# Optimization experiments

Hardware: AMD Instinct MI355X
Metric: run time of the kernel (lower is better)

Reference implementation:

```python
import jax, jax.numpy as jnp
import numpy as np

N_NODES = 100000
N_EDGES = 600000
IN_SIZE = 128
NUM_HEADS = 8
OUT_DIM = 16  # out_size // num_heads = 128 // 8
NEG_SLOPE = 0.2


def setup_inputs() -> dict:
    key = jax.random.key(0)
    k1, k2, k3, k4, k5, k6, k7 = jax.random.split(key, 7)
    h = jax.random.normal(k1, (N_NODES, IN_SIZE), dtype=jnp.float32)
    o = jax.random.normal(k2, (N_NODES, NUM_HEADS * OUT_DIM), dtype=jnp.float32)
    # scale params for numerical sanity of exp() in edge softmax
    W = jax.random.normal(k3, (IN_SIZE, NUM_HEADS * OUT_DIM), dtype=jnp.float32) * 0.05
    attn_l = jax.random.normal(k4, (NUM_HEADS, OUT_DIM), dtype=jnp.float32) * 0.05
    attn_r = jax.random.normal(k5, (NUM_HEADS, OUT_DIM), dtype=jnp.float32) * 0.05
    src = jax.random.randint(k6, (N_EDGES,), 0, N_NODES, dtype=jnp.int64)
    dst = jax.random.randint(k7, (N_EDGES,), 0, N_NODES, dtype=jnp.int64)
    return {"h": h, "o": o, "W": W, "attn_l": attn_l, "attn_r": attn_r,
            "src": src, "dst": dst}


def reference(h, o, W, attn_l, attn_r, src, dst):
    N = h.shape[0]
    # linear projection -> per-head features [N, H, D]
    z = (h @ W).reshape(N, NUM_HEADS, OUT_DIM)
    # per-node attention logit halves [N, H]
    el = jnp.einsum('nhd,hd->nh', z, attn_l)
    er = jnp.einsum('nhd,hd->nh', z, attn_r)
    # per-edge score: message src -> dst, LeakyReLU  [E, H]
    e = jax.nn.leaky_relu(el[dst] + er[src], negative_slope=NEG_SLOPE)
    # edge softmax over incoming edges of each destination node
    m = jax.ops.segment_max(e, dst, num_segments=N)          # [N, H]
    ex = jnp.exp(e - m[dst])                                  # [E, H]
    s = jax.ops.segment_sum(ex, dst, num_segments=N)          # [N, H]
    alpha = ex / s[dst]                                       # [E, H]
    # weighted aggregate of source features  [N, H, D]
    msg = alpha[:, :, None] * z[src]                          # [E, H, D]
    agg = jax.ops.segment_sum(msg, dst, num_segments=N)
    # merge='cat' -> [N, H*D]; residual + ELU
    out = agg.reshape(N, NUM_HEADS * OUT_DIM)
    return o + jax.nn.elu(out)
```

## Files before the change

kernel.cpp:

```cpp
#include <hip/hip_runtime.h>
#include <hip/hip_bf16.h>
#include <math.h>

#define NNODES 100000
#define NEDGES 600000
#define IN 128
#define HD 128
#define NH 8
#define NEG_SLOPE 0.2f
#define LOG2E 1.44269504f
#define RG_TOTAL (NNODES / 16)
#define NFRAG 36
#define CT_ALL 9
#define NPAD 100352
#define SCAN_BLOCKS 98
#define PACK_BLOCKS 9
#define HIST4_BLOCKS ((NEDGES / 4 + 255) / 256)
#define GEMM_BLOCKS 782

typedef __attribute__((ext_vector_type(8))) short short8v;
typedef __attribute__((ext_vector_type(4))) float f32x4;

__device__ inline unsigned short f2bf(float f) {
    unsigned u = __float_as_uint(f);
    unsigned r = (u + 0x7fff + ((u >> 16) & 1)) >> 16;
    return (unsigned short)r;
}
__device__ inline float bflo(unsigned v) { return __uint_as_float(v << 16); }
__device__ inline float bfhi(unsigned v) { return __uint_as_float(v & 0xffff0000u); }
__device__ inline unsigned cvtpk(float lo, float hi) {
    unsigned r;
    asm("v_cvt_pk_bf16_f32 %0, %1, %2" : "=v"(r) : "v"(lo), "v"(hi));
    return r;
}

__global__ __launch_bounds__(256) void k_pack_hist(
    const float* __restrict__ W, const float* __restrict__ attn_l, const float* __restrict__ attn_r,
    short8v* __restrict__ Wb,
    const int* __restrict__ dst, int* __restrict__ cnt, int* __restrict__ rank)
{
    const int tid = threadIdx.x;
    if (blockIdx.x < PACK_BLOCKS) {
        int slot = blockIdx.x * 256 + tid;
        int f = slot >> 6, lane = slot & 63;
        int ks = f / CT_ALL, ct = f % CT_ALL;
        int k0 = ks * 32 + (lane >> 4) * 8;
        short8v v;
        if (ct < 8) {
            int col = ct * 16 + (lane & 15);
            #pragma unroll
            for (int j = 0; j < 8; ++j) v[j] = (short)f2bf(W[(k0 + j) * HD + col]);
        } else {
            int c = lane & 15;
            const float* av = (c < 8) ? attn_l : attn_r;
            int hh = c & 7;
            #pragma unroll
            for (int j = 0; j < 8; ++j) {
                int k = k0 + j;
                float s = 0.f;
                for (int d = 0; d < 16; ++d) s += W[k * HD + hh * 16 + d] * av[hh * 16 + d];
                v[j] = (short)f2bf(s * LOG2E);
            }
        }
        Wb[slot] = v;
    } else {
        int e0 = ((blockIdx.x - PACK_BLOCKS) * 256 + tid) * 4;
        if (e0 < NEDGES) {
            int4 d4 = *(const int4*)(dst + e0);
            int4 r4;
            r4.x = atomicAdd(&cnt[d4.x], 1);
            r4.y = atomicAdd(&cnt[d4.y], 1);
            r4.z = atomicAdd(&cnt[d4.z], 1);
            r4.w = atomicAdd(&cnt[d4.w], 1);
            *(int4*)(rank + e0) = r4;
        }
    }
}

__global__ __launch_bounds__(256) void k_gemm_scan1(
    const float* __restrict__ h, const short8v* __restrict__ Wb,
    unsigned short* __restrict__ z, float* __restrict__ el, float* __restrict__ er,
    const int* __restrict__ cnt, int* __restrict__ inc, int* __restrict__ bsum)
{
    __shared__ short8v Bs[NFRAG * 64];
    __shared__ int sd[2][256];
    const int tid = threadIdx.x;

    if (blockIdx.x < SCAN_BLOCKS) {
        int gid4 = blockIdx.x * 256 + tid;
        int4 v = ((const int4*)cnt)[gid4];
        int s1 = v.x + v.y, s2 = s1 + v.z, s3 = s2 + v.w;
        sd[0][tid] = s3; __syncthreads();
        int cur = 0;
        for (int off = 1; off < 256; off <<= 1) {
            int nv = sd[cur][tid] + (tid >= off ? sd[cur][tid - off] : 0);
            sd[cur ^ 1][tid] = nv; __syncthreads();
            cur ^= 1;
        }
        int incl = sd[cur][tid];
        int eb = incl - s3;
        int4 w = make_int4(eb + v.x, eb + s1, eb + s2, eb + s3);
        ((int4*)inc)[gid4] = w;
        if (tid == 255) bsum[blockIdx.x] = incl;
        return;
    }

    {
        const float4* srcp = (const float4*)Wb;
        float4* dstp = (float4*)Bs;
        for (int i = tid; i < NFRAG * 64; i += 256) dstp[i] = srcp[i];
    }
    __syncthreads();

    const int lane  = tid & 63;
    const int rowIn = lane & 15;
    const int kgrp  = lane >> 4;
    int wid = ((blockIdx.x - SCAN_BLOCKS) * 256 + tid) >> 6;
    const int nw = GEMM_BLOCKS * 4;

    for (int rg = wid; rg < RG_TOTAL; rg += nw) {
        const int row0 = rg * 16;
        const float* hp = h + (size_t)(row0 + rowIn) * IN + kgrp * 8;

        short8v afr[4];
        #pragma unroll
        for (int ks = 0; ks < 4; ++ks) {
            float4 a0 = *(const float4*)(hp + ks * 32);
            float4 a1 = *(const float4*)(hp + ks * 32 + 4);
            uint4 u;
            u.x = cvtpk(a0.x, a0.y);
            u.y = cvtpk(a0.z, a0.w);
            u.z = cvtpk(a1.x, a1.y);
            u.w = cvtpk(a1.z, a1.w);
            afr[ks] = __builtin_bit_cast(short8v, u);
        }

        f32x4 acc[CT_ALL];
        #pragma unroll
        for (int ct = 0; ct < CT_ALL; ++ct) acc[ct] = (f32x4){0.f, 0.f, 0.f, 0.f};

        #pragma unroll
        for (int ks = 0; ks < 4; ++ks)
            #pragma unroll
            for (int ct = 0; ct < CT_ALL; ++ct)
                acc[ct] = __builtin_amdgcn_mfma_f32_16x16x32_bf16(
                    Bs[(ks * CT_ALL + ct) * 64 + lane], afr[ks], acc[ct], 0, 0, 0);

        const size_t zrow = (size_t)(row0 + rowIn) * HD;
        #pragma unroll
        for (int ct = 0; ct < 8; ++ct) {
            uint2 pk;
            pk.x = cvtpk(acc[ct][0], acc[ct][1]);
            pk.y = cvtpk(acc[ct][2], acc[ct][3]);
            *(uint2*)(z + zrow + ct * 16 + kgrp * 4) = pk;
        }
        {
            float4 v = make_float4(acc[8][0], acc[8][1], acc[8][2], acc[8][3]);
            int row = row0 + rowIn;
            if (kgrp < 2) *(float4*)(el + row * NH + kgrp * 4) = v;
            else          *(float4*)(er + row * NH + (kgrp - 2) * 4) = v;
        }
    }
}

__global__ __launch_bounds__(256) void kscan23(
    const int* __restrict__ cnt, const int* __restrict__ inc, const int* __restrict__ bsum,
    int* __restrict__ offs)
{
    __shared__ int bs[2][128];
    const int tid = threadIdx.x;
    if (tid < 128) bs[0][tid] = (tid < SCAN_BLOCKS) ? bsum[tid] : 0;
    __syncthreads();
    int cur = 0;
    for (int off = 1; off < 128; off <<= 1) {
        if (tid < 128) {
            int nv = bs[cur][tid] + (tid >= off ? bs[cur][tid - off] : 0);
            bs[cur ^ 1][tid] = nv;
        }
        __syncthreads();
        cur ^= 1;
    }
    const int base = (blockIdx.x == 0) ? 0 : bs[cur][blockIdx.x - 1];

    int gid4 = blockIdx.x * 256 + tid;
    int4 c = ((const int4*)cnt)[gid4];
    int4 ic = ((const int4*)inc)[gid4];
    int i0 = gid4 * 4;
    int ex[4] = { base + ic.x - c.x, base + ic.y - c.y, base + ic.z - c.z, base + ic.w - c.w };
    #pragma unroll
    for (int j = 0; j < 4; ++j) {
        int i = i0 + j;
        if (i < NNODES) offs[i] = ex[j];
        else if (i == NNODES) offs[i] = NEDGES;
    }
}

__global__ void k_scatter(const int* __restrict__ src, const int* __restrict__ dst,
                          const int* __restrict__ rank, const int* __restrict__ offs,
                          int* __restrict__ esrc) {
    int e0 = (blockIdx.x * blockDim.x + threadIdx.x) * 4;
    if (e0 >= NEDGES) return;
    int4 s4 = *(const int4*)(src + e0);
    int4 d4 = *(const int4*)(dst + e0);
    int4 r4 = *(const int4*)(rank + e0);
    esrc[offs[d4.x] + r4.x] = s4.x;
    esrc[offs[d4.y] + r4.y] = s4.y;
    esrc[offs[d4.z] + r4.z] = s4.z;
    esrc[offs[d4.w] + r4.w] = s4.w;
}

__global__ __launch_bounds__(256) void k_agg(
    const int* __restrict__ offs, const int* __restrict__ esrc,
    const float* __restrict__ el, const float* __restrict__ er,
    const unsigned short* __restrict__ z, const float* __restrict__ o,
    float* __restrict__ out)
{
    const int wid  = (blockIdx.x * blockDim.x + threadIdx.x) >> 6;
    const int lane = threadIdx.x & 63;
    if (wid >= NNODES) return;
    const int d  = wid;
    const int p0 = offs[d];
    const int n  = offs[d + 1] - p0;
    const int g  = lane & 31;
    const int e2 = lane >> 5;
    const int hh = g >> 2;
    const float el8 = el[d * NH + hh];

    const size_t obase = (size_t)d * HD + g * 4;
    const f32x4 ov = __builtin_nontemporal_load((const f32x4*)(o + obase));

    float srun = 0.f;
    f32x4 acc = (f32x4){0.f, 0.f, 0.f, 0.f};

    for (int c0 = 0; c0 < n; c0 += 64) {
        const int m = (n - c0 < 64) ? (n - c0) : 64;
        int sid = __builtin_nontemporal_load(esrc + p0 + c0 + (lane < m ? lane : 0));

        for (int b = 0; b < m; b += 8) {
            float erv[4]; uint2 zb[4];
            #pragma unroll
            for (int k = 0; k < 4; ++k) {
                int ei = b + k * 2 + e2;
                int eic = (ei < m) ? ei : 0;
                int s = __shfl(sid, eic, 64);
                erv[k] = er[s * NH + hh];
                zb[k]  = *(const uint2*)(z + (size_t)s * HD + g * 4);
            }
            #pragma unroll
            for (int k = 0; k < 4; ++k) {
                int ei = b + k * 2 + e2;
                float ev = el8 + erv[k];
                ev = fmaxf(ev, NEG_SLOPE * ev);
                float ex = (ei < m) ? __builtin_exp2f(ev) : 0.f;
                srun += ex;
                acc[0] = fmaf(ex, bflo(zb[k].x), acc[0]);
                acc[1] = fmaf(ex, bfhi(zb[k].x), acc[1]);
                acc[2] = fmaf(ex, bflo(zb[k].y), acc[2]);
                acc[3] = fmaf(ex, bfhi(zb[k].y), acc[3]);
            }
        }
    }

    srun   += __shfl_xor(srun, 32, 64);
    acc[0] += __shfl_xor(acc[0], 32, 64);
    acc[1] += __shfl_xor(acc[1], 32, 64);
    acc[2] += __shfl_xor(acc[2], 32, 64);
    acc[3] += __shfl_xor(acc[3], 32, 64);

    if (lane < 32) {
        float inv = (srun > 0.f) ? 1.f / srun : 0.f;
        float r0 = acc[0] * inv, r1 = acc[1] * inv, r2 = acc[2] * inv, r3 = acc[3] * inv;
        r0 = (r0 > 0.f) ? r0 : expm1f(r0);
        r1 = (r1 > 0.f) ? r1 : expm1f(r1);
        r2 = (r2 > 0.f) ? r2 : expm1f(r2);
        r3 = (r3 > 0.f) ? r3 : expm1f(r3);
        f32x4 res = (f32x4){ov[0] + r0, ov[1] + r1, ov[2] + r2, ov[3] + r3};
        __builtin_nontemporal_store(res, (f32x4*)(out + obase));
    }
}

extern "C" void kernel_launch(void* const* d_in, const int* in_sizes, int n_in,
                              void* d_out, int out_size, void* d_ws, size_t ws_size,
                              hipStream_t stream) {
    const float* h      = (const float*)d_in[0];
    const float* o      = (const float*)d_in[1];
    const float* W      = (const float*)d_in[2];
    const float* attn_l = (const float*)d_in[3];
    const float* attn_r = (const float*)d_in[4];
    const int*   src    = (const int*)d_in[5];
    const int*   dst    = (const int*)d_in[6];
    float* out = (float*)d_out;

    char* ws = (char*)d_ws;
    unsigned short* z = (unsigned short*)(ws);
    float* el     = (float*)(ws + 25600000);
    float* er     = (float*)(ws + 28800000);
    int*   cnt    = (int*)  (ws + 32000000);
    int*   inc    = (int*)  (ws + 32401408);
    int*   offs   = (int*)  (ws + 32802816);
    int*   rank   = (int*)  (ws + 33202832);
    int*   bsum   = (int*)  (ws + 35602832);
    int*   esrc   = (int*)  (ws + 35603344);
    short8v* Wb   = (short8v*)(ws + 38003344);

    hipMemsetAsync(cnt, 0, NPAD * sizeof(int), stream);

    k_pack_hist<<<PACK_BLOCKS + HIST4_BLOCKS, 256, 0, stream>>>(W, attn_l, attn_r, Wb, dst, cnt, rank);
    k_gemm_scan1<<<SCAN_BLOCKS + GEMM_BLOCKS, 256, 0, stream>>>(h, Wb, z, el, er, cnt, inc, bsum);
    kscan23<<<SCAN_BLOCKS, 256, 0, stream>>>(cnt, inc, bsum, offs);
    k_scatter<<<(NEDGES / 4 + 255) / 256, 256, 0, stream>>>(src, dst, rank, offs, esrc);
    k_agg<<<(NNODES * 64 + 255) / 256, 256, 0, stream>>>(offs, esrc, el, er, z, o, out);
}
```

Before: 123.4 us.

## Process four destination nodes per wavefront with interleaved gather pipelining

The aggregation kernel now assigns four consecutive destination nodes to each wavefront instead of one. It loads their edge lists in one batch and software-pipelines the per-node gathers of er and z, issuing the next node's loads before consuming the current one. The aim is to keep more memory requests in flight per wave and amortize offset and index loads, hiding gather latency for low-degree nodes (about 6 edges on average). The cost is more registers, a loop bound set by the maximum degree among the four nodes, and fewer waves in total.

```diff
diff --git a/kernel.cpp b/kernel.cpp
--- a/kernel.cpp
+++ b/kernel.cpp
@@ -215,68 +215,114 @@
     const unsigned short* __restrict__ z, const float* __restrict__ o,
     float* __restrict__ out)
 {
-    const int wid  = (blockIdx.x * blockDim.x + threadIdx.x) >> 6;
+    const int wv   = (blockIdx.x * blockDim.x + threadIdx.x) >> 6;
     const int lane = threadIdx.x & 63;
-    if (wid >= NNODES) return;
-    const int d  = wid;
-    const int p0 = offs[d];
-    const int n  = offs[d + 1] - p0;
+    const int d0   = wv * 4;
+    if (d0 >= NNODES) return;
     const int g  = lane & 31;
     const int e2 = lane >> 5;
     const int hh = g >> 2;
-    const float el8 = el[d * NH + hh];
-
-    const size_t obase = (size_t)d * HD + g * 4;
-    const f32x4 ov = __builtin_nontemporal_load((const f32x4*)(o + obase));
-
-    float srun = 0.f;
-    f32x4 acc = (f32x4){0.f, 0.f, 0.f, 0.f};
-
-    for (int c0 = 0; c0 < n; c0 += 64) {
-        const int m = (n - c0 < 64) ? (n - c0) : 64;
-        int sid = __builtin_nontemporal_load(esrc + p0 + c0 + (lane < m ? lane : 0));
-
-        for (int b = 0; b < m; b += 8) {
-            float erv[4]; uint2 zb[4];
-            #pragma unroll
-            for (int k = 0; k < 4; ++k) {
-                int ei = b + k * 2 + e2;
-                int eic = (ei < m) ? ei : 0;
-                int s = __shfl(sid, eic, 64);
-                erv[k] = er[s * NH + hh];
-                zb[k]  = *(const uint2*)(z + (size_t)s * HD + g * 4);
-            }
-            #pragma unroll
-            for (int k = 0; k < 4; ++k) {
-                int ei = b + k * 2 + e2;
-                float ev = el8 + erv[k];
-                ev = fmaxf(ev, NEG_SLOPE * ev);
-                float ex = (ei < m) ? __builtin_exp2f(ev) : 0.f;
-                srun += ex;
-                acc[0] = fmaf(ex, bflo(zb[k].x), acc[0]);
-                acc[1] = fmaf(ex, bfhi(zb[k].x), acc[1]);
-                acc[2] = fmaf(ex, bflo(zb[k].y), acc[2]);
-                acc[3] = fmaf(ex, bfhi(zb[k].y), acc[3]);
-            }
-        }
-    }
-
-    srun   += __shfl_xor(srun, 32, 64);
-    acc[0] += __shfl_xor(acc[0], 32, 64);
-    acc[1] += __shfl_xor(acc[1], 32, 64);
-    acc[2] += __shfl_xor(acc[2], 32, 64);
-    acc[3] += __shfl_xor(acc[3], 32, 64);
-
-    if (lane < 32) {
-        float inv = (srun > 0.f) ? 1.f / srun : 0.f;
-        float r0 = acc[0] * inv, r1 = acc[1] * inv, r2 = acc[2] * inv, r3 = acc[3] * inv;
-        r0 = (r0 > 0.f) ? r0 : expm1f(r0);
-        r1 = (r1 > 0.f) ? r1 : expm1f(r1);
-        r2 = (r2 > 0.f) ? r2 : expm1f(r2);
-        r3 = (r3 > 0.f) ? r3 : expm1f(r3);
-        f32x4 res = (f32x4){ov[0] + r0, ov[1] + r1, ov[2] + r2, ov[3] + r3};
-        __builtin_nontemporal_store(res, (f32x4*)(out + obase));
-    }
+    const int q   = lane >> 4;
+    const int l15 = lane & 15;
+
+    int po[5];
+    #pragma unroll
+    for (int j = 0; j < 5; ++j) po[j] = offs[d0 + j];
+    const int n0 = po[1] - po[0], n1 = po[2] - po[1], n2 = po[3] - po[2], n3 = po[4] - po[3];
+    const int p_q = (q == 0) ? po[0] : (q == 1) ? po[1] : (q == 2) ? po[2] : po[3];
+    const int n_q = (q == 0) ? n0 : (q == 1) ? n1 : (q == 2) ? n2 : n3;
+
+    const float el0 = el[(d0 + 0) * NH + hh];
+    const float el1 = el[(d0 + 1) * NH + hh];
+    const float el2 = el[(d0 + 2) * NH + hh];
+    const float el3 = el[(d0 + 3) * NH + hh];
+
+    float sr0 = 0.f, sr1 = 0.f, sr2 = 0.f, sr3 = 0.f;
+    f32x4 a0 = (f32x4){0.f,0.f,0.f,0.f}, a1 = a0, a2 = a0, a3 = a0;
+
+    int nmax = n0 > n1 ? n0 : n1;
+    nmax = nmax > n2 ? nmax : n2;
+    nmax = nmax > n3 ? nmax : n3;
+
+    float ervA[4], ervB[4];
+    uint2 zbA[4], zbB[4];
+
+    for (int c0 = 0; c0 < nmax; c0 += 8) {
+        int off_in = c0 + ((l15 < 8) ? l15 : 0);
+        if (off_in >= n_q) off_in = (n_q > 0) ? (n_q - 1) : 0;
+        int idx = p_q + off_in;
+        if (idx > NEDGES - 1) idx = NEDGES - 1;
+        const int sid = __builtin_nontemporal_load(esrc + idx);
+
+#define ISSUE(J, NJ, ERV, ZB) if (c0 < NJ) { \
+            int mj = NJ - c0; if (mj > 8) mj = 8; \
+            _Pragma("unroll") \
+            for (int k = 0; k < 4; ++k) { \
+                int sl = k * 2 + e2; \
+                int slc = (sl < mj) ? sl : 0; \
+                int s = __shfl(sid, (J) * 16 + slc, 64); \
+                ERV[k] = er[s * NH + hh]; \
+                ZB[k] = *(const uint2*)(z + (size_t)s * HD + g * 4); \
+            } }
+
+#define CONSUME(J, NJ, ELJ, SR, AC, ERV, ZB) if (c0 < NJ) { \
+            int mj = NJ - c0; if (mj > 8) mj = 8; \
+            _Pragma("unroll") \
+            for (int k = 0; k < 4; ++k) { \
+                int sl = k * 2 + e2; \
+                float ev = ELJ + ERV[k]; \
+                ev = fmaxf(ev, NEG_SLOPE * ev); \
+                float ex = (sl < mj) ? __builtin_exp2f(ev) : 0.f; \
+                SR += ex; \
+                AC[0] = fmaf(ex, bflo(ZB[k].x), AC[0]); \
+                AC[1] = fmaf(ex, bfhi(ZB[k].x), AC[1]); \
+                AC[2] = fmaf(ex, bflo(ZB[k].y), AC[2]); \
+                AC[3] = fmaf(ex, bfhi(ZB[k].y), AC[3]); \
+            } }
+
+        ISSUE(0, n0, ervA, zbA)
+        ISSUE(1, n1, ervB, zbB)
+        CONSUME(0, n0, el0, sr0, a0, ervA, zbA)
+        ISSUE(2, n2, ervA, zbA)
+        CONSUME(1, n1, el1, sr1, a1, ervB, zbB)
+        ISSUE(3, n3, ervB, zbB)
+        CONSUME(2, n2, el2, sr2, a2, ervA, zbA)
+        CONSUME(3, n3, el3, sr3, a3, ervB, zbB)
+#undef ISSUE
+#undef CONSUME
+    }
+
+    const size_t ob0 = (size_t)(d0 + 0) * HD + g * 4;
+    const size_t ob1 = (size_t)(d0 + 1) * HD + g * 4;
+    const size_t ob2 = (size_t)(d0 + 2) * HD + g * 4;
+    const size_t ob3 = (size_t)(d0 + 3) * HD + g * 4;
+    const f32x4 ov0 = __builtin_nontemporal_load((const f32x4*)(o + ob0));
+    const f32x4 ov1 = __builtin_nontemporal_load((const f32x4*)(o + ob1));
+    const f32x4 ov2 = __builtin_nontemporal_load((const f32x4*)(o + ob2));
+    const f32x4 ov3 = __builtin_nontemporal_load((const f32x4*)(o + ob3));
+
+#define EPI(SR, AC, OV, OB) { \
+        SR += __shfl_xor(SR, 32, 64); \
+        AC[0] += __shfl_xor(AC[0], 32, 64); \
+        AC[1] += __shfl_xor(AC[1], 32, 64); \
+        AC[2] += __shfl_xor(AC[2], 32, 64); \
+        AC[3] += __shfl_xor(AC[3], 32, 64); \
+        if (lane < 32) { \
+            float inv = (SR > 0.f) ? 1.f / SR : 0.f; \
+            float r0 = AC[0]*inv, r1 = AC[1]*inv, r2 = AC[2]*inv, r3 = AC[3]*inv; \
+            r0 = (r0 > 0.f) ? r0 : expm1f(r0); \
+            r1 = (r1 > 0.f) ? r1 : expm1f(r1); \
+            r2 = (r2 > 0.f) ? r2 : expm1f(r2); \
+            r3 = (r3 > 0.f) ? r3 : expm1f(r3); \
+            f32x4 res = (f32x4){OV[0]+r0, OV[1]+r1, OV[2]+r2, OV[3]+r3}; \
+            __builtin_nontemporal_store(res, (f32x4*)(out + OB)); \
+        } }
+
+    EPI(sr0, a0, ov0, ob0)
+    EPI(sr1, a1, ov1, ob1)
+    EPI(sr2, a2, ov2, ob2)
+    EPI(sr3, a3, ov3, ob3)
+#undef EPI
 }
 
 extern "C" void kernel_launch(void* const* d_in, const int* in_sizes, int n_in,
@@ -309,5 +355,5 @@
     k_gemm_scan1<<<SCAN_BLOCKS + GEMM_BLOCKS, 256, 0, stream>>>(h, Wb, z, el, er, cnt, inc, bsum);
     kscan23<<<SCAN_BLOCKS, 256, 0, stream>>>(cnt, inc, bsum, offs);
     k_scatter<<<(NEDGES / 4 + 255) / 256, 256, 0, stream>>>(src, dst, rank, offs, esrc);
-    k_agg<<<(NNODES * 64 + 255) / 256, 256, 0, stream>>>(offs, esrc, el, er, z, o, out);
-}
+    k_agg<<<NNODES / 16, 256, 0, stream>>>(offs, esrc, el, er, z, o, out);
+}
```

Result: slower. 133.8 us (+8.4%).
